# Kernel tuning notes

Measured on AMD Instinct MI355X. Metric: run time of the kernel, lower is better.

Reference implementation:

```python
import jax, jax.numpy as jnp
import numpy as np
from functools import partial

B, S, V, H, NH, NKV, M, L = 2, 2048, 51200, 1536, 24, 4, 8960, 8
DH = H // NH  # 64
EPS = 1e-6


def setup_inputs() -> dict:
    key = jax.random.key(0)
    ks = jax.random.split(key, 16)
    sc = 0.02
    w = lambda k, shape: jax.random.normal(k, shape, jnp.float32) * sc
    inp = {
        "input_ids": jax.random.randint(ks[0], (B, S), 0, V),
        "attention_mask": jnp.ones((B, S), jnp.float32),
        "embed": w(ks[1], (V, H)),
        "Wq": w(ks[2], (L, H, H)),          "bq": jnp.zeros((L, H), jnp.float32),
        "Wk": w(ks[3], (L, H, NKV * DH)),   "bk": jnp.zeros((L, NKV * DH), jnp.float32),
        "Wv": w(ks[4], (L, H, NKV * DH)),   "bv": jnp.zeros((L, NKV * DH), jnp.float32),
        "Wo": w(ks[5], (L, H, H)),
        "ln1": jnp.ones((L, H), jnp.float32),
        "ln2": jnp.ones((L, H), jnp.float32),
        "Wg": w(ks[6], (L, H, M)),
        "Wu": w(ks[7], (L, H, M)),
        "Wd": w(ks[8], (L, M, H)),
        "norm_w": jnp.ones((H,), jnp.float32),
        "W1": w(ks[9], (H, H)), "b1": jnp.zeros((H,), jnp.float32),
        "W2": w(ks[10], (H, 1)), "b2": jnp.zeros((1,), jnp.float32),
    }
    inv_freq = 1.0 / (10000.0 ** (jnp.arange(0, DH, 2, dtype=jnp.float32) / DH))
    freqs = jnp.outer(jnp.arange(S, dtype=jnp.float32), inv_freq)  # [S, DH/2]
    emb = jnp.concatenate([freqs, freqs], axis=-1)                 # [S, DH]
    inp["cos"] = jnp.cos(emb)
    inp["sin"] = jnp.sin(emb)
    return inp


def _rms(x, w):
    var = jnp.mean(x.astype(jnp.float32) ** 2, axis=-1, keepdims=True)
    return w * (x * jax.lax.rsqrt(var + EPS)).astype(x.dtype)


def _rotate_half(x):
    x1, x2 = jnp.split(x, 2, axis=-1)
    return jnp.concatenate([-x2, x1], axis=-1)


def _forward(input_ids, attention_mask, embed, Wq, bq, Wk, bk, Wv, bv, Wo,
             ln1, ln2, Wg, Wu, Wd, norm_w, W1, b1, W2, b2, cos, sin):
    scale = 1.0 / np.sqrt(DH)
    b, s = input_ids.shape
    c = cos[None, :s, None, :]  # [1,S,1,DH]
    sn = sin[None, :s, None, :]
    rope = lambda t: t * c + _rotate_half(t) * sn
    mask0 = attention_mask[:, None, None, :] == 0  # [B,1,1,S]

    def block(x, p):
        wq, bq_, wk, bk_, wv, bv_, wo, ln1w, ln2w, wg, wu, wd = p
        h = _rms(x, ln1w)
        q = (h @ wq + bq_).reshape(b, s, NH, DH)
        k = (h @ wk + bk_).reshape(b, s, NKV, DH)
        v = (h @ wv + bv_).reshape(b, s, NKV, DH)
        q, k = rope(q), rope(k)
        k = jnp.repeat(k, NH // NKV, axis=2)  # GQA expand to NH heads
        v = jnp.repeat(v, NH // NKV, axis=2)
        scores = jnp.einsum('bqhd,bkhd->bhqk', q, k) * scale
        scores = jnp.where(mask0, -1e10, scores)
        probs = jax.nn.softmax(scores, axis=-1)  # dropout: eval mode (identity)
        attn = jnp.einsum('bhqk,bkhd->bqhd', probs, v).reshape(b, s, H)
        x = x + attn @ wo
        h = _rms(x, ln2w)
        x = x + (jax.nn.sigmoid(h @ wg) * (h @ wu)) @ wd
        return x, None

    x = embed[input_ids]  # [B,S,H]
    x, _ = jax.lax.scan(block, x, (Wq, bq, Wk, bk, Wv, bv, Wo, ln1, ln2, Wg, Wu, Wd))
    x = _rms(x, norm_w)
    h = jax.nn.gelu(x @ W1 + b1, approximate=False)  # torch nn.GELU default = exact
    return h @ W2 + b2  # [B,S,1]


def reference(input_ids, attention_mask, embed, Wq, bq, Wk, bk, Wv, bv, Wo,
              ln1, ln2, Wg, Wu, Wd, norm_w, W1, b1, W2, b2, cos, sin):
    return _forward(input_ids, attention_mask, embed, Wq, bq, Wk, bk, Wv, bv, Wo,
                    ln1, ln2, Wg, Wu, Wd, norm_w, W1, b1, W2, b2, cos, sin)
```

## Files before the change

### kernel.cpp

```cpp
#include <hip/hip_runtime.h>

typedef float f32x4 __attribute__((ext_vector_type(4)));
typedef short s16x8 __attribute__((ext_vector_type(8)));
typedef unsigned short u16;
typedef unsigned short u16x4 __attribute__((ext_vector_type(4)));
typedef unsigned short u16x8 __attribute__((ext_vector_type(8)));

__device__ __forceinline__ float bf2f(u16 u){ union{unsigned int i; float f;} v; v.i=((unsigned int)u)<<16; return v.f; }
__device__ __forceinline__ u16 f2bf(float f){ union{float f; unsigned int i;} v; v.f=f; return (u16)((v.i + 0x7FFFu + ((v.i>>16)&1u))>>16); }

__device__ __forceinline__ void gld16(const void* gp, void* lp){
  __builtin_amdgcn_global_load_lds((__attribute__((address_space(1))) void*)(void*)gp,
                                   (__attribute__((address_space(3))) void*)lp, 16, 0, 0);
}

__global__ __launch_bounds__(256) void k_embed(const int* __restrict__ ids, const float* __restrict__ emb, float* __restrict__ x){
  int r = blockIdx.x;
  int id = ids[r];
  const f32x4* src = (const f32x4*)(emb + (size_t)id*1536);
  f32x4* dst = (f32x4*)(x + (size_t)r*1536);
  for (int i = threadIdx.x; i < 384; i += 256) dst[i] = src[i];
}

__global__ __launch_bounds__(256) void k_rms(const float* __restrict__ x, const float* __restrict__ w, u16* __restrict__ h){
  int r = blockIdx.x, tid = threadIdx.x;
  const f32x4* xr = (const f32x4*)(x + (size_t)r*1536);
  f32x4 v0 = xr[tid];
  float ss = v0.x*v0.x + v0.y*v0.y + v0.z*v0.z + v0.w*v0.w;
  f32x4 v1 = {0,0,0,0};
  if (tid < 128){ v1 = xr[256+tid]; ss += v1.x*v1.x + v1.y*v1.y + v1.z*v1.z + v1.w*v1.w; }
  #pragma unroll
  for (int off=32; off; off>>=1) ss += __shfl_xor(ss, off, 64);
  __shared__ float red[4];
  if ((tid&63)==0) red[tid>>6] = ss;
  __syncthreads();
  float tot = red[0]+red[1]+red[2]+red[3];
  float invr = rsqrtf(tot*(1.f/1536.f) + 1e-6f);
  const f32x4* w4 = (const f32x4*)w;
  u16x4* h4 = (u16x4*)(h + (size_t)r*1536);
  {
    f32x4 wv = w4[tid];
    u16x4 o; o.x=f2bf(v0.x*invr*wv.x); o.y=f2bf(v0.y*invr*wv.y); o.z=f2bf(v0.z*invr*wv.z); o.w=f2bf(v0.w*invr*wv.w);
    h4[tid] = o;
  }
  if (tid < 128){
    f32x4 wv = w4[256+tid];
    u16x4 o; o.x=f2bf(v1.x*invr*wv.x); o.y=f2bf(v1.y*invr*wv.y); o.z=f2bf(v1.z*invr*wv.z); o.w=f2bf(v1.w*invr*wv.w);
    h4[256+tid] = o;
  }
}

__global__ __launch_bounds__(256) void k_rms_add(float* __restrict__ x, const float* __restrict__ P, const float* __restrict__ w, u16* __restrict__ h){
  int r = blockIdx.x, tid = threadIdx.x;
  f32x4* xr = (f32x4*)(x + (size_t)r*1536);
  const f32x4* pr = (const f32x4*)(P + (size_t)r*1536);
  f32x4 v0 = xr[tid], p0 = pr[tid];
  v0.x+=p0.x; v0.y+=p0.y; v0.z+=p0.z; v0.w+=p0.w;
  xr[tid] = v0;
  float ss = v0.x*v0.x + v0.y*v0.y + v0.z*v0.z + v0.w*v0.w;
  f32x4 v1 = {0,0,0,0};
  if (tid < 128){
    v1 = xr[256+tid]; f32x4 p1 = pr[256+tid];
    v1.x+=p1.x; v1.y+=p1.y; v1.z+=p1.z; v1.w+=p1.w;
    xr[256+tid] = v1;
    ss += v1.x*v1.x + v1.y*v1.y + v1.z*v1.z + v1.w*v1.w;
  }
  #pragma unroll
  for (int off=32; off; off>>=1) ss += __shfl_xor(ss, off, 64);
  __shared__ float red[4];
  if ((tid&63)==0) red[tid>>6] = ss;
  __syncthreads();
  float tot = red[0]+red[1]+red[2]+red[3];
  float invr = rsqrtf(tot*(1.f/1536.f) + 1e-6f);
  const f32x4* w4 = (const f32x4*)w;
  u16x4* h4 = (u16x4*)(h + (size_t)r*1536);
  {
    f32x4 wv = w4[tid];
    u16x4 o; o.x=f2bf(v0.x*invr*wv.x); o.y=f2bf(v0.y*invr*wv.y); o.z=f2bf(v0.z*invr*wv.z); o.w=f2bf(v0.w*invr*wv.w);
    h4[tid] = o;
  }
  if (tid < 128){
    f32x4 wv = w4[256+tid];
    u16x4 o; o.x=f2bf(v1.x*invr*wv.x); o.y=f2bf(v1.y*invr*wv.y); o.z=f2bf(v1.z*invr*wv.z); o.w=f2bf(v1.w*invr*wv.w);
    h4[256+tid] = o;
  }
}

__device__ __forceinline__ void cvt_tile(const float* src, int K, int N, u16* dst, int k0, int n0, int roff, int mode){
  __shared__ float T[64*72];
  int tid = threadIdx.x;
  #pragma unroll
  for (int j=0;j<4;++j){
    int i = tid + j*256;
    int row = i>>4, nf = i&15;
    f32x4 vv = *(const f32x4*)(src + (size_t)(k0+row)*N + n0 + nf*4);
    *(f32x4*)&T[row*72 + nf*4] = vv;
  }
  __syncthreads();
  #pragma unroll
  for (int j=0;j<2;++j){
    int i = tid + j*256;
    int n = i>>3, kc = i&7;
    u16x8 o;
    #pragma unroll
    for (int m=0;m<8;++m) o[m] = f2bf(T[(kc*8+m)*72 + n]);
    int gn = n0 + n;
    int dr = (mode==0) ? (roff + gn) : (((gn>>4)<<5) + ((mode==2)?16:0) + (gn&15));
    *(u16x8*)(dst + (size_t)dr*K + k0 + kc*8) = o;
  }
}

__global__ __launch_bounds__(256) void k_cvt_layer(
  const float* __restrict__ Wq, const float* __restrict__ Wk, const float* __restrict__ Wv,
  const float* __restrict__ Wo, const float* __restrict__ Wg, const float* __restrict__ Wu,
  const float* __restrict__ Wd, u16* qkvt, u16* wot, u16* gut, u16* wdt)
{
  const float* src; int K, N; u16* dst; int roff=0, mode=0;
  switch (blockIdx.y){
    case 0: src=Wq; K=1536; N=1536; dst=qkvt; break;
    case 1: src=Wk; K=1536; N=256;  dst=qkvt; roff=1536; break;
    case 2: src=Wv; K=1536; N=256;  dst=qkvt; roff=1792; break;
    case 3: src=Wo; K=1536; N=1536; dst=wot;  break;
    case 4: src=Wg; K=1536; N=8960; dst=gut;  mode=1; break;
    case 5: src=Wu; K=1536; N=8960; dst=gut;  mode=2; break;
    default: src=Wd; K=8960; N=1536; dst=wdt; break;
  }
  int ntn = N>>6;
  int nt = (K>>6)*ntn;
  int t = blockIdx.x;
  if (t >= nt) return;
  cvt_tile(src, K, N, dst, (t/ntn)<<6, (t%ntn)<<6, roff, mode);
}

__global__ __launch_bounds__(256) void k_cvt_one(const float* __restrict__ src, u16* __restrict__ dst){
  int t = blockIdx.x;
  cvt_tile(src, 1536, 1536, dst, (t/24)<<6, (t%24)<<6, 0, 0);
}

#define MODE_QKV 0
#define MODE_WO 1
#define MODE_GATEUP 2
#define MODE_DOWN 3
#define MODE_W1 4

template<int MODE>
__global__ __launch_bounds__(256) void k_gemm(
  const u16* __restrict__ A, const u16* __restrict__ Bt, int K,
  int jobsPerXcd, int nc, int ksplit, int klen,
  const float* __restrict__ bq_, const float* __restrict__ bk_, const float* __restrict__ bv_,
  float* __restrict__ xio, float* __restrict__ Pf,
  const float* __restrict__ cosT, const float* __restrict__ sinT,
  u16* __restrict__ o0, u16* __restrict__ o1, u16* __restrict__ o2)
{
  int bid = blockIdx.x;
  int xcd = bid & 7, j = bid >> 3;
  int job = xcd*jobsPerXcd + (j >> 5);
  if (job >= nc*ksplit) return;
  int rowb = j & 31;
  int col = job / ksplit;
  int ks  = job - col*ksplit;
  int kbase = ks*klen;

  __shared__ u16 As[4096], Bs[4096];
  int tid = threadIdx.x;
  int lane = tid & 63, w = tid >> 6;
  int wr = w >> 1, wc = w & 1;
  int row0 = rowb * 128, col0 = col * 128;
  int l15 = lane & 15, l4 = lane >> 4;
  f32x4 acc[4][4] = {};
  const u16* aBase = A + (size_t)row0*K;
  const u16* bBase = Bt + (size_t)col0*K;
  int rr0 = tid & 127, kb0 = tid >> 7;
  int kb1 = kb0 + 2;
  for (int kt = kbase; kt < kbase+klen; kt += 32){
    gld16(aBase + (size_t)rr0*K + kt + kb0*8, &As[tid*8]);
    gld16(bBase + (size_t)rr0*K + kt + kb0*8, &Bs[tid*8]);
    gld16(aBase + (size_t)rr0*K + kt + kb1*8, &As[(256+tid)*8]);
    gld16(bBase + (size_t)rr0*K + kt + kb1*8, &Bs[(256+tid)*8]);
    __syncthreads();
    s16x8 af[4], bf_[4];
    #pragma unroll
    for (int i=0;i<4;++i) af[i]  = *(const s16x8*)&As[((l4<<7) + wr*64 + i*16 + l15)*8];
    #pragma unroll
    for (int jj=0;jj<4;++jj) bf_[jj] = *(const s16x8*)&Bs[((l4<<7) + wc*64 + jj*16 + l15)*8];
    #pragma unroll
    for (int i=0;i<4;++i)
      #pragma unroll
      for (int jj=0;jj<4;++jj)
        acc[i][jj] = __builtin_amdgcn_mfma_f32_16x16x32_bf16(af[i], bf_[jj], acc[i][jj], 0, 0, 0);
    __syncthreads();
  }
  #pragma unroll
  for (int i=0;i<4;++i)
    #pragma unroll
    for (int jj=0;jj<4;++jj)
      #pragma unroll
      for (int r=0;r<4;++r){
        int row = row0 + wr*64 + i*16 + l4*4 + r;
        int c   = col0 + wc*64 + jj*16 + l15;
        float v = acc[i][jj][r];
        if constexpr (MODE == MODE_QKV){
          int b = row >> 11, s = row & 2047;
          if (c < 1536){
            int d = c & 63, hd = c >> 6;
            float vv = v + bq_[c];
            float pv = acc[i][jj^2][r] + bq_[c^32];
            float cv = cosT[s*64+d], sv = sinT[s*64+d];
            float sgn = (d<32) ? -1.f : 1.f;
            float o = (vv*cv + sgn*pv*sv)*0.125f;
            o0[(size_t)(b*24+hd)*131072 + (size_t)(s>>6)*4096 + (d>>3)*512 + (s&63)*8 + (d&7)] = f2bf(o);
          } else if (c < 1792){
            int c2 = c - 1536, d = c2 & 63, kv = c2 >> 6;
            float vv = v + bk_[c2];
            float pv = acc[i][jj^2][r] + bk_[c2^32];
            float cv = cosT[s*64+d], sv = sinT[s*64+d];
            float sgn = (d<32) ? -1.f : 1.f;
            float o = vv*cv + sgn*pv*sv;
            o1[(size_t)(b*4+kv)*131072 + (size_t)(s>>6)*4096 + (d>>3)*512 + (s&63)*8 + (d&7)] = f2bf(o);
          } else {
            int c2 = c - 1792, d = c2 & 63, kv = c2 >> 6;
            float vv = v + bv_[c2];
            o2[(size_t)(b*4+kv)*131072 + (size_t)(s>>3)*512 + d*8 + (s&7)] = f2bf(vv);
          }
        } else if constexpr (MODE == MODE_WO){
          xio[(size_t)row*1536 + c] += v;
        } else if constexpr (MODE == MODE_W1){
          v += bq_[c];
          float ge = 0.5f * v * (1.f + erff(v * 0.70710678118f));
          o0[(size_t)row*1536 + c] = f2bf(ge);
        }
      }
}

template<int MODE>
__global__ __launch_bounds__(512,2) void k_gemm256(
  const u16* __restrict__ A, const u16* __restrict__ Bt, int K,
  int nrt, int ksplit, int klen,
  float* __restrict__ xio, float* __restrict__ Pf, u16* __restrict__ o0)
{
  int bid = blockIdx.x;
  int wgid = (bid & 7)*(gridDim.x >> 3) + (bid >> 3);
  int nj = nrt*ksplit;
  int ct = wgid / nj; int r2 = wgid - ct*nj;
  int rt = r2 / ksplit; int ks = r2 - rt*ksplit;

  __shared__ __align__(16) u16 lds[2][2][16384];
  int tid = threadIdx.x;
  int lane = tid & 63, wid = tid >> 6;
  int wm = wid >> 2, wn = wid & 3;
  int l15 = lane & 15, l4 = lane >> 4;
  int row0 = rt*256, col0 = ct*256;
  int kbase = ks*klen*64;

  const u16* aB = A  + (size_t)row0*K + kbase;
  const u16* bB = Bt + (size_t)col0*K + kbase;
  int rsub = tid >> 3;
  int gsw  = (lane & 7) ^ ((lane >> 3) & 7);

  f32x4 acc[8][4] = {};

  auto stage = [&](int bf, int ktElem){
    #pragma unroll
    for (int a_=0; a_<4; ++a_){
      gld16(aB + (size_t)(a_*64 + rsub)*K + ktElem + gsw*8, &lds[bf][0][(a_*512+tid)*8]);
      gld16(bB + (size_t)(a_*64 + rsub)*K + ktElem + gsw*8, &lds[bf][1][(a_*512+tid)*8]);
    }
  };

  stage(0, 0);
  for (int t = 0; t < klen; ++t){
    asm volatile("s_waitcnt vmcnt(0)" ::: "memory");
    __builtin_amdgcn_s_barrier();
    __builtin_amdgcn_sched_barrier(0);
    if (t+1 < klen) stage((t+1)&1, (t+1)*64);
    const u16* Ab = lds[t&1][0];
    const u16* Bb = lds[t&1][1];
    #pragma unroll
    for (int ksu=0; ksu<2; ++ksu){
      s16x8 af[8], bf_[4];
      #pragma unroll
      for (int i=0;i<8;++i){
        int r = wm*128 + i*16 + l15;
        af[i] = *(const s16x8*)&Ab[r*64 + (((ksu*4 + l4) ^ (l15&7))*8)];
      }
      #pragma unroll
      for (int j=0;j<4;++j){
        int c = wn*64 + j*16 + l15;
        bf_[j] = *(const s16x8*)&Bb[c*64 + (((ksu*4 + l4) ^ (l15&7))*8)];
      }
      #pragma unroll
      for (int i=0;i<8;++i)
        #pragma unroll
        for (int j=0;j<4;++j)
          acc[i][j] = __builtin_amdgcn_mfma_f32_16x16x32_bf16(af[i], bf_[j], acc[i][j], 0, 0, 0);
    }
  }

  if constexpr (MODE == MODE_GATEUP){
    #pragma unroll
    for (int i=0;i<8;++i)
      #pragma unroll
      for (int j2=0;j2<4;j2+=2)
        #pragma unroll
        for (int r=0;r<4;++r){
          int row = row0 + wm*128 + i*16 + l4*4 + r;
          int cp  = col0 + wn*64 + j2*16 + l15;
          float gv = acc[i][j2][r], uv = acc[i][j2+1][r];
          float sg = 1.f/(1.f + __expf(-gv));
          int n = ((cp>>5)<<4) + (cp&15);
          o0[(size_t)row*8960 + n] = f2bf(sg*uv);
        }
  } else {
    #pragma unroll
    for (int i=0;i<8;++i)
      #pragma unroll
      for (int j=0;j<4;++j)
        #pragma unroll
        for (int r=0;r<4;++r){
          int row = row0 + wm*128 + i*16 + l4*4 + r;
          int c   = col0 + wn*64 + j*16 + l15;
          float v = acc[i][j][r];
          if (ks == 0) Pf[(size_t)row*1536 + c] = v;
          else         xio[(size_t)row*1536 + c] += v;
        }
  }
}

#define MFIX 4.0f
__global__ __launch_bounds__(256) void k_attn(
  const u16* __restrict__ q, const u16* __restrict__ k, const u16* __restrict__ v,
  const float* __restrict__ mask, u16* __restrict__ attn)
{
  __shared__ __align__(16) u16 Qs[4096];
  __shared__ __align__(16) u16 Kd[2][4096];
  __shared__ __align__(16) u16 Vd[2][4096];
  __shared__ __align__(16) u16 Ps[4][1024];
  __shared__ u16 Msh[2048];
  int tid = threadIdx.x;
  int lane = tid & 63, w = tid >> 6;
  int qb = blockIdx.x;
  int bh = blockIdx.y;
  int b = bh / 24, hh = bh % 24, kv = hh / 6;
  int l15 = lane & 15, l4 = lane >> 4;

  const u16* qhead = q + ((size_t)(b*24 + hh))*131072 + qb*4096;
  const u16* khead = k + ((size_t)(b*4  + kv))*131072;
  const u16* vhead = v + ((size_t)(b*4  + kv))*131072;

  {
    const f32x4* m4 = (const f32x4*)(mask + b*2048);
    for (int i = tid; i < 512; i += 256){
      f32x4 mv = m4[i];
      u16x4 o;
      o.x = f2bf(mv.x==0.f ? -1e9f : 0.f);
      o.y = f2bf(mv.y==0.f ? -1e9f : 0.f);
      o.z = f2bf(mv.z==0.f ? -1e9f : 0.f);
      o.w = f2bf(mv.w==0.f ? -1e9f : 0.f);
      *(u16x4*)&Msh[i*4] = o;
    }
  }
  gld16(qhead + tid*8,       &Qs[tid*8]);
  gld16(qhead + (256+tid)*8, &Qs[(256+tid)*8]);

  auto stage = [&](int bf, int kt){
    gld16(khead + kt*4096 + tid*8,       &Kd[bf][tid*8]);
    gld16(khead + kt*4096 + (256+tid)*8, &Kd[bf][(256+tid)*8]);
    gld16(vhead + kt*4096 + tid*8,       &Vd[bf][tid*8]);
    gld16(vhead + kt*4096 + (256+tid)*8, &Vd[bf][(256+tid)*8]);
  };
  stage(0, 0);

  s16x8 aq0, aq1;
  f32x4 oacc[4] = {};
  float lsum[4] = {0.f,0.f,0.f,0.f};

  for (int t = 0; t < 32; ++t){
    asm volatile("s_waitcnt vmcnt(0)" ::: "memory");
    __builtin_amdgcn_s_barrier();
    __builtin_amdgcn_sched_barrier(0);
    if (t == 0){
      aq0 = *(const s16x8*)&Qs[(( l4   *64) + w*16 + l15)*8];
      aq1 = *(const s16x8*)&Qs[(((4+l4)*64) + w*16 + l15)*8];
    }
    if (t+1 < 32) stage((t+1)&1, t+1);
    const u16* Kb = Kd[t&1];
    const u16* Vb = Vd[t&1];
    f32x4 sk[4] = {};
    #pragma unroll
    for (int kn=0; kn<4; ++kn){
      s16x8 bk0 = *(const s16x8*)&Kb[(( l4   *64) + kn*16 + l15)*8];
      s16x8 bk1 = *(const s16x8*)&Kb[(((4+l4)*64) + kn*16 + l15)*8];
      sk[kn] = __builtin_amdgcn_mfma_f32_16x16x32_bf16(aq0, bk0, sk[kn], 0,0,0);
      sk[kn] = __builtin_amdgcn_mfma_f32_16x16x32_bf16(aq1, bk1, sk[kn], 0,0,0);
    }
    #pragma unroll
    for (int kn=0; kn<4; ++kn){
      float mb = bf2f(Msh[t*64 + kn*16 + l15]);
      int kk = kn*16 + l15;
      #pragma unroll
      for (int r=0;r<4;++r){
        float p = __expf(sk[kn][r] + mb - MFIX);
        lsum[r] += p;
        Ps[w][((kk>>3)*16 + l4*4 + r)*8 + (kk&7)] = f2bf(p);
      }
    }
    #pragma unroll
    for (int ksu=0; ksu<2; ++ksu){
      s16x8 ap = *(const s16x8*)&Ps[w][((ksu*4+l4)*16 + l15)*8];
      #pragma unroll
      for (int dg=0; dg<4; ++dg){
        s16x8 bv = *(const s16x8*)&Vb[((ksu*4+l4)*64 + dg*16 + l15)*8];
        oacc[dg] = __builtin_amdgcn_mfma_f32_16x16x32_bf16(ap, bv, oacc[dg], 0,0,0);
      }
    }
  }
  #pragma unroll
  for (int r=0;r<4;++r){
    float t = lsum[r];
    t += __shfl_xor(t, 1, 64); t += __shfl_xor(t, 2, 64);
    t += __shfl_xor(t, 4, 64); t += __shfl_xor(t, 8, 64);
    lsum[r] = 1.f / t;
  }
  #pragma unroll
  for (int dg=0;dg<4;++dg)
    #pragma unroll
    for (int r=0;r<4;++r){
      int token = b*2048 + qb*64 + w*16 + l4*4 + r;
      int col = hh*64 + dg*16 + l15;
      attn[(size_t)token*1536 + col] = f2bf(oacc[dg][r] * lsum[r]);
    }
}

__global__ __launch_bounds__(256) void k_gemv(const u16* __restrict__ h2, const float* __restrict__ W2, const float* __restrict__ b2, float* __restrict__ out){
  int tid = threadIdx.x, lane = tid & 63, w = tid >> 6;
  int r = blockIdx.x*4 + w;
  const u16* hr = h2 + (size_t)r*1536;
  float s = 0.f;
  #pragma unroll
  for (int i=0;i<24;++i){ int c = lane + i*64; s += bf2f(hr[c]) * W2[c]; }
  #pragma unroll
  for (int off=32; off; off>>=1) s += __shfl_xor(s, off, 64);
  if (lane == 0) out[r] = s + b2[0];
}

extern "C" void kernel_launch(void* const* d_in, const int* in_sizes, int n_in,
                              void* d_out, int out_size, void* d_ws, size_t ws_size,
                              hipStream_t stream)
{
  const int*   ids   = (const int*)d_in[0];
  const float* mask  = (const float*)d_in[1];
  const float* embed = (const float*)d_in[2];
  const float* Wq    = (const float*)d_in[3];
  const float* bq    = (const float*)d_in[4];
  const float* Wk    = (const float*)d_in[5];
  const float* bk    = (const float*)d_in[6];
  const float* Wv    = (const float*)d_in[7];
  const float* bv    = (const float*)d_in[8];
  const float* Wo    = (const float*)d_in[9];
  const float* ln1   = (const float*)d_in[10];
  const float* ln2   = (const float*)d_in[11];
  const float* Wg    = (const float*)d_in[12];
  const float* Wu    = (const float*)d_in[13];
  const float* Wd    = (const float*)d_in[14];
  const float* nw    = (const float*)d_in[15];
  const float* W1    = (const float*)d_in[16];
  const float* b1    = (const float*)d_in[17];
  const float* W2    = (const float*)d_in[18];
  const float* b2    = (const float*)d_in[19];
  const float* cosT  = (const float*)d_in[20];
  const float* sinT  = (const float*)d_in[21];

  char* ws = (char*)d_ws;
  float* x   = (float*)(ws + 0);
  u16* h     = (u16*)(ws + 25165824);
  u16* qb_   = (u16*)(ws + 37748736);
  u16* kb_   = (u16*)(ws + 50331648);
  u16* vb_   = (u16*)(ws + 52428800);
  u16* attn  = (u16*)(ws + 54525952);
  u16* g     = (u16*)(ws + 67108864);
  u16* qkvt  = (u16*)(ws + 140509184);
  u16* wot   = (u16*)(ws + 146800640);
  u16* gut   = (u16*)(ws + 151519232);
  u16* wdt   = (u16*)(ws + 206569472);
  float* Pf  = (float*)(ws + 37748736);
  (void)in_sizes; (void)n_in; (void)out_size; (void)ws_size;

  k_embed<<<4096, 256, 0, stream>>>(ids, embed, x);
  for (int l = 0; l < 8; ++l){
    k_cvt_layer<<<dim3(3360,7), 256, 0, stream>>>(
      Wq + (size_t)l*1536*1536, Wk + (size_t)l*1536*256, Wv + (size_t)l*1536*256,
      Wo + (size_t)l*1536*1536, Wg + (size_t)l*1536*8960, Wu + (size_t)l*1536*8960,
      Wd + (size_t)l*8960*1536, qkvt, wot, gut, wdt);
    if (l == 0) k_rms<<<4096, 256, 0, stream>>>(x, ln1, h);
    else        k_rms_add<<<4096, 256, 0, stream>>>(x, Pf, ln1 + l*1536, h);
    k_gemm<MODE_QKV><<<512, 256, 0, stream>>>(h, qkvt, 1536, 2, 16, 1, 1536,
        bq + l*1536, bk + l*256, bv + l*256, nullptr, nullptr, cosT, sinT, qb_, kb_, vb_);
    k_attn<<<dim3(32,48), 256, 0, stream>>>(qb_, kb_, vb_, mask, attn);
    k_gemm<MODE_WO><<<512, 256, 0, stream>>>(attn, wot, 1536, 2, 12, 1, 1536,
        nullptr, nullptr, nullptr, x, nullptr, nullptr, nullptr, nullptr, nullptr, nullptr);
    k_rms<<<4096, 256, 0, stream>>>(x, ln2 + l*1536, h);
    k_gemm256<MODE_GATEUP><<<1120, 512, 0, stream>>>(h, gut, 1536, 16, 1, 24,
        nullptr, nullptr, g);
    k_gemm256<MODE_DOWN><<<192, 512, 0, stream>>>(g, wdt, 8960, 16, 2, 70,
        x, Pf, nullptr);
  }
  k_cvt_one<<<576, 256, 0, stream>>>(W1, wot);
  k_rms_add<<<4096, 256, 0, stream>>>(x, Pf, nw, h);
  k_gemm<MODE_W1><<<512, 256, 0, stream>>>(h, wot, 1536, 2, 12, 1, 1536,
      b1, nullptr, nullptr, nullptr, nullptr, nullptr, nullptr, attn, nullptr, nullptr);
  k_gemv<<<1024, 256, 0, stream>>>(attn, W2, b2, (float*)d_out);
}
```

Measured before the change: 5.699 ms.

## Deepen LDS prefetch pipelines in small GEMM and attention, add MFMA priority hints

The 128x128 GEMM moves from a single LDS buffer with two syncthreads per k-step to a 4-stage ring that prefetches three tiles ahead, using vmcnt waits in place of full barriers. The attention kernel goes from double to triple buffering of K/V tiles, with a partial vmcnt wait. s_setprio raises wave priority around MFMA blocks in all three kernels. The aim is to hide global-load latency behind compute, at the cost of more LDS, which may reduce occupancy.

After: 5.698 ms. No clear change (-0.0%).

```diff
diff --git a/kernel.cpp b/kernel.cpp
--- a/kernel.cpp
+++ b/kernel.cpp
@@ -160,8 +160,9 @@
   int col = job / ksplit;
   int ks  = job - col*ksplit;
   int kbase = ks*klen;
-
-  __shared__ u16 As[4096], Bs[4096];
+  int nt = klen >> 5;
+
+  __shared__ __align__(16) u16 As[4][4096], Bs[4][4096];
   int tid = threadIdx.x;
   int lane = tid & 63, w = tid >> 6;
   int wr = w >> 1, wc = w & 1;
@@ -172,24 +173,38 @@
   const u16* bBase = Bt + (size_t)col0*K;
   int rr0 = tid & 127, kb0 = tid >> 7;
   int kb1 = kb0 + 2;
-  for (int kt = kbase; kt < kbase+klen; kt += 32){
-    gld16(aBase + (size_t)rr0*K + kt + kb0*8, &As[tid*8]);
-    gld16(bBase + (size_t)rr0*K + kt + kb0*8, &Bs[tid*8]);
-    gld16(aBase + (size_t)rr0*K + kt + kb1*8, &As[(256+tid)*8]);
-    gld16(bBase + (size_t)rr0*K + kt + kb1*8, &Bs[(256+tid)*8]);
-    __syncthreads();
+
+  auto stage = [&](int bf, int kt){
+    gld16(aBase + (size_t)rr0*K + kt + kb0*8, &As[bf][tid*8]);
+    gld16(bBase + (size_t)rr0*K + kt + kb0*8, &Bs[bf][tid*8]);
+    gld16(aBase + (size_t)rr0*K + kt + kb1*8, &As[bf][(256+tid)*8]);
+    gld16(bBase + (size_t)rr0*K + kt + kb1*8, &Bs[bf][(256+tid)*8]);
+  };
+  stage(0, kbase); stage(1, kbase+32); stage(2, kbase+64);
+
+  for (int t = 0; t < nt; ++t){
+    if (t < nt-2)       asm volatile("s_waitcnt vmcnt(8)" ::: "memory");
+    else if (t == nt-2) asm volatile("s_waitcnt vmcnt(4)" ::: "memory");
+    else                asm volatile("s_waitcnt vmcnt(0)" ::: "memory");
+    __builtin_amdgcn_s_barrier();
+    __builtin_amdgcn_sched_barrier(0);
+    if (t+3 < nt) stage((t+3)&3, kbase + (t+3)*32);
+    const u16* Ab = As[t&3];
+    const u16* Bb = Bs[t&3];
     s16x8 af[4], bf_[4];
     #pragma unroll
-    for (int i=0;i<4;++i) af[i]  = *(const s16x8*)&As[((l4<<7) + wr*64 + i*16 + l15)*8];
-    #pragma unroll
-    for (int jj=0;jj<4;++jj) bf_[jj] = *(const s16x8*)&Bs[((l4<<7) + wc*64 + jj*16 + l15)*8];
+    for (int i=0;i<4;++i) af[i]  = *(const s16x8*)&Ab[((l4<<7) + wr*64 + i*16 + l15)*8];
+    #pragma unroll
+    for (int jj=0;jj<4;++jj) bf_[jj] = *(const s16x8*)&Bb[((l4<<7) + wc*64 + jj*16 + l15)*8];
+    __builtin_amdgcn_s_setprio(1);
     #pragma unroll
     for (int i=0;i<4;++i)
       #pragma unroll
       for (int jj=0;jj<4;++jj)
         acc[i][jj] = __builtin_amdgcn_mfma_f32_16x16x32_bf16(af[i], bf_[jj], acc[i][jj], 0, 0, 0);
-    __syncthreads();
-  }
+    __builtin_amdgcn_s_setprio(0);
+  }
+
   #pragma unroll
   for (int i=0;i<4;++i)
     #pragma unroll
@@ -288,11 +303,13 @@
         int c = wn*64 + j*16 + l15;
         bf_[j] = *(const s16x8*)&Bb[c*64 + (((ksu*4 + l4) ^ (l15&7))*8)];
       }
+      __builtin_amdgcn_s_setprio(1);
       #pragma unroll
       for (int i=0;i<8;++i)
         #pragma unroll
         for (int j=0;j<4;++j)
           acc[i][j] = __builtin_amdgcn_mfma_f32_16x16x32_bf16(af[i], bf_[j], acc[i][j], 0, 0, 0);
+      __builtin_amdgcn_s_setprio(0);
     }
   }
 
@@ -332,8 +349,8 @@
   const float* __restrict__ mask, u16* __restrict__ attn)
 {
   __shared__ __align__(16) u16 Qs[4096];
-  __shared__ __align__(16) u16 Kd[2][4096];
-  __shared__ __align__(16) u16 Vd[2][4096];
+  __shared__ __align__(16) u16 Kd[3][4096];
+  __shared__ __align__(16) u16 Vd[3][4096];
   __shared__ __align__(16) u16 Ps[4][1024];
   __shared__ u16 Msh[2048];
   int tid = threadIdx.x;
@@ -369,23 +386,26 @@
     gld16(vhead + kt*4096 + (256+tid)*8, &Vd[bf][(256+tid)*8]);
   };
   stage(0, 0);
+  stage(1, 1);
 
   s16x8 aq0, aq1;
   f32x4 oacc[4] = {};
   float lsum[4] = {0.f,0.f,0.f,0.f};
 
   for (int t = 0; t < 32; ++t){
-    asm volatile("s_waitcnt vmcnt(0)" ::: "memory");
+    if (t < 31) asm volatile("s_waitcnt vmcnt(4)" ::: "memory");
+    else        asm volatile("s_waitcnt vmcnt(0)" ::: "memory");
     __builtin_amdgcn_s_barrier();
     __builtin_amdgcn_sched_barrier(0);
     if (t == 0){
       aq0 = *(const s16x8*)&Qs[(( l4   *64) + w*16 + l15)*8];
       aq1 = *(const s16x8*)&Qs[(((4+l4)*64) + w*16 + l15)*8];
     }
-    if (t+1 < 32) stage((t+1)&1, t+1);
-    const u16* Kb = Kd[t&1];
-    const u16* Vb = Vd[t&1];
+    if (t+2 < 32) stage((t+2)%3, t+2);
+    const u16* Kb = Kd[t%3];
+    const u16* Vb = Vd[t%3];
     f32x4 sk[4] = {};
+    __builtin_amdgcn_s_setprio(1);
     #pragma unroll
     for (int kn=0; kn<4; ++kn){
       s16x8 bk0 = *(const s16x8*)&Kb[(( l4   *64) + kn*16 + l15)*8];
@@ -393,6 +413,7 @@
       sk[kn] = __builtin_amdgcn_mfma_f32_16x16x32_bf16(aq0, bk0, sk[kn], 0,0,0);
       sk[kn] = __builtin_amdgcn_mfma_f32_16x16x32_bf16(aq1, bk1, sk[kn], 0,0,0);
     }
+    __builtin_amdgcn_s_setprio(0);
     #pragma unroll
     for (int kn=0; kn<4; ++kn){
       float mb = bf2f(Msh[t*64 + kn*16 + l15]);
@@ -404,6 +425,7 @@
         Ps[w][((kk>>3)*16 + l4*4 + r)*8 + (kk&7)] = f2bf(p);
       }
     }
+    __builtin_amdgcn_s_setprio(1);
     #pragma unroll
     for (int ksu=0; ksu<2; ++ksu){
       s16x8 ap = *(const s16x8*)&Ps[w][((ksu*4+l4)*16 + l15)*8];
@@ -413,6 +435,7 @@
         oacc[dg] = __builtin_amdgcn_mfma_f32_16x16x32_bf16(ap, bv, oacc[dg], 0,0,0);
       }
     }
+    __builtin_amdgcn_s_setprio(0);
   }
   #pragma unroll
   for (int r=0;r<4;++r){
```
